# Kernel optimization log

Measured on AMD Instinct MI355X. Metric: run time of the kernel, lower is better.

Reference implementation:

```python
import jax, jax.numpy as jnp
import numpy as np

B, L, H, NH, NB = 16, 200, 128, 2, 2
ITEMS, SPAN = 50000, 256
NEG = -2.0**32 + 1.0  # mask value used by the torch module


def _ln(x, g, b, eps=1e-8):
    m = jnp.mean(x, axis=-1, keepdims=True)
    v = jnp.mean((x - m) ** 2, axis=-1, keepdims=True)
    return (x - m) / jnp.sqrt(v + eps) * g + b


def setup_inputs() -> dict:
    key = jax.random.key(0)
    ks = jax.random.split(key, 20)
    p = lambda k, s: (jax.random.normal(k, s, jnp.float32) * 0.02)
    item_emb = p(ks[0], (ITEMS + 1, H)).at[0].set(0.0)  # padding_idx=0
    return {
        "user_ids": jax.random.randint(ks[1], (B,), 0, 10000),
        "log_seqs": jax.random.randint(ks[2], (B, L), 0, ITEMS),
        "time_matrices": jax.random.randint(ks[3], (B, L, L), 0, SPAN),
        "pos_seqs": jax.random.randint(ks[4], (B, L), 0, ITEMS),
        "neg_seqs": jax.random.randint(ks[5], (B, L), 0, ITEMS),
        "item_emb": item_emb,
        "pos_K_emb": p(ks[6], (L, H)),
        "pos_V_emb": p(ks[7], (L, H)),
        "time_K_emb": p(ks[8], (SPAN + 1, H)),
        "time_V_emb": p(ks[9], (SPAN + 1, H)),
        "Wq": p(ks[10], (NB, H, H)), "bq": jnp.zeros((NB, H)),
        "Wk": p(ks[11], (NB, H, H)), "bk": jnp.zeros((NB, H)),
        "Wv": p(ks[12], (NB, H, H)), "bv": jnp.zeros((NB, H)),
        "ln1_g": jnp.ones((NB, H)), "ln1_b": jnp.zeros((NB, H)),
        "W1": p(ks[13], (NB, H, H)), "b1": jnp.zeros((NB, H)),
        "W2": p(ks[14], (NB, H, H)), "b2": jnp.zeros((NB, H)),
        "ln2_g": jnp.ones((NB, H)), "ln2_b": jnp.zeros((NB, H)),
        "lnf_g": jnp.ones((H,)), "lnf_b": jnp.zeros((H,)),
    }


def reference(user_ids, log_seqs, time_matrices, pos_seqs, neg_seqs,
              item_emb, pos_K_emb, pos_V_emb, time_K_emb, time_V_emb,
              Wq, bq, Wk, bk, Wv, bv, ln1_g, ln1_b,
              W1, b1, W2, b2, ln2_g, ln2_b, lnf_g, lnf_b):
    d = H // NH
    pad = (log_seqs == 0)                    # (B,L) timeline mask
    keep = (~pad)[..., None].astype(jnp.float32)

    seqs = item_emb[log_seqs] * jnp.sqrt(jnp.float32(H))
    seqs = seqs * keep
    posK = pos_K_emb.reshape(L, NH, d)       # same for every batch element
    posV = pos_V_emb.reshape(L, NH, d)
    tmK = time_K_emb[time_matrices].reshape(B, L, L, NH, d)  # (B,L,L,h,d)
    tmV = time_V_emb[time_matrices].reshape(B, L, L, NH, d)
    causal = ~jnp.tril(jnp.ones((L, L), dtype=bool))          # True = masked
    mask = pad[:, None, :, None] | causal[None, None, :, :]   # (B,1,L,L) row-mask | causal

    for i in range(NB):
        Q = (seqs @ Wq[i].T + bq[i]).reshape(B, L, NH, d)
        K = (seqs @ Wk[i].T + bk[i]).reshape(B, L, NH, d)
        V = (seqs @ Wv[i].T + bv[i]).reshape(B, L, NH, d)
        aw = jnp.einsum('bqhd,bkhd->bhqk', Q, K)
        aw = aw + jnp.einsum('bqhd,khd->bhqk', Q, posK)
        aw = aw + jnp.einsum('bqkhd,bqhd->bhqk', tmK, Q)
        aw = aw / jnp.sqrt(jnp.float32(d))
        aw = jnp.where(mask, NEG, aw)
        A = jax.nn.softmax(aw, axis=-1)                        # (B,h,L,L)
        out = jnp.einsum('bhqk,bkhd->bqhd', A, V)
        out = out + jnp.einsum('bhqk,khd->bqhd', A, posV)
        out = out + jnp.einsum('bhqk,bqkhd->bqhd', A, tmV)
        out = out.reshape(B, L, H)
        seqs = _ln(seqs + out, ln1_g[i], ln1_b[i])
        ffn = jax.nn.relu(seqs @ W1[i].T + b1[i]) @ W2[i].T + b2[i]
        seqs = _ln(seqs + ffn, ln2_g[i], ln2_b[i])
        seqs = seqs * keep

    log_feats = _ln(seqs, lnf_g, lnf_b)
    pos_logits = jnp.sum(log_feats * item_emb[pos_seqs], axis=-1)  # (B,L)
    neg_logits = jnp.sum(log_feats * item_emb[neg_seqs], axis=-1)
    return jnp.stack([pos_logits, neg_logits])  # (2,B,L)
```

## Files before the change

### kernel.cpp

```cpp
#include <hip/hip_runtime.h>
#include <hip/hip_bf16.h>
#include <math.h>

#define BB 16
#define LL 200
#define HH 128
#define DD 64
#define NQT 25
#define NEGF -4294967295.0f
#define SQRTH 11.313708498984761f
#define WSTR 129

__device__ __forceinline__ void stage_w(const float* __restrict__ W,
                                        float* __restrict__ w_lds, int t) {
#pragma unroll
    for (int i = 0; i < 8; ++i) {
        int x = t + i * 512;
        int c = x >> 5, k4 = x & 31;
        float4 v = ((const float4*)W)[x];
        float* dst = w_lds + c * WSTR + k4 * 4;
        dst[0] = v.x; dst[1] = v.y; dst[2] = v.z; dst[3] = v.w;
    }
}

__device__ __forceinline__ float wsum64(float v) {
    v += __shfl_xor(v, 1, 64);  v += __shfl_xor(v, 2, 64);
    v += __shfl_xor(v, 4, 64);  v += __shfl_xor(v, 8, 64);
    v += __shfl_xor(v, 16, 64); v += __shfl_xor(v, 32, 64);
    return v;
}

__global__ __launch_bounds__(512) void k_qkv(float* __restrict__ seqs,
    const int* __restrict__ log_seqs, const float* __restrict__ item_emb,
    const float* __restrict__ Wq, const float* __restrict__ bq,
    const float* __restrict__ Wk, const float* __restrict__ bk,
    const float* __restrict__ Wv, const float* __restrict__ bv,
    const float* __restrict__ posK, const float* __restrict__ posV,
    float* __restrict__ Q, float* __restrict__ Kp, float* __restrict__ Vp) {
    __shared__ float s_lds[8][HH];
    __shared__ float w_lds[HH * WSTR];
    int r0g = blockIdx.x * 8;
    int t = threadIdx.x;
    if (t < 256) {
        int r = t >> 5, d4 = t & 31;
        int id = log_seqs[r0g + r];
        float4 v = make_float4(0.f, 0.f, 0.f, 0.f);
        if (id != 0) {
            v = ((const float4*)(item_emb + id * HH))[d4];
            v.x *= SQRTH; v.y *= SQRTH; v.z *= SQRTH; v.w *= SQRTH;
        }
        *(float4*)&s_lds[r][d4 * 4] = v;
        ((float4*)(seqs + r0g * HH))[t] = v;
    }
    stage_w(Wq, w_lds, t);
    __syncthreads();
    int c = t & 127, rg = t >> 7;
    const float* wrow = w_lds + c * WSTR;
    float a0, a1;
    a0 = 0.f; a1 = 0.f;
#pragma unroll 4
    for (int k4 = 0; k4 < 32; ++k4) {
        float w0 = wrow[k4 * 4 + 0], w1 = wrow[k4 * 4 + 1];
        float w2 = wrow[k4 * 4 + 2], w3 = wrow[k4 * 4 + 3];
        float4 s0 = *(const float4*)&s_lds[rg * 2][k4 * 4];
        float4 s1 = *(const float4*)&s_lds[rg * 2 + 1][k4 * 4];
        a0 += s0.x * w0 + s0.y * w1 + s0.z * w2 + s0.w * w3;
        a1 += s1.x * w0 + s1.y * w1 + s1.z * w2 + s1.w * w3;
    }
    Q[(r0g + rg * 2) * HH + c]     = a0 + bq[c];
    Q[(r0g + rg * 2 + 1) * HH + c] = a1 + bq[c];
    __syncthreads();
    stage_w(Wk, w_lds, t);
    __syncthreads();
    a0 = 0.f; a1 = 0.f;
#pragma unroll 4
    for (int k4 = 0; k4 < 32; ++k4) {
        float w0 = wrow[k4 * 4 + 0], w1 = wrow[k4 * 4 + 1];
        float w2 = wrow[k4 * 4 + 2], w3 = wrow[k4 * 4 + 3];
        float4 s0 = *(const float4*)&s_lds[rg * 2][k4 * 4];
        float4 s1 = *(const float4*)&s_lds[rg * 2 + 1][k4 * 4];
        a0 += s0.x * w0 + s0.y * w1 + s0.z * w2 + s0.w * w3;
        a1 += s1.x * w0 + s1.y * w1 + s1.z * w2 + s1.w * w3;
    }
    {
        int row0 = r0g + rg * 2, row1 = row0 + 1;
        Kp[row0 * HH + c] = a0 + bk[c] + posK[(row0 % LL) * HH + c];
        Kp[row1 * HH + c] = a1 + bk[c] + posK[(row1 % LL) * HH + c];
    }
    __syncthreads();
    stage_w(Wv, w_lds, t);
    __syncthreads();
    a0 = 0.f; a1 = 0.f;
#pragma unroll 4
    for (int k4 = 0; k4 < 32; ++k4) {
        float w0 = wrow[k4 * 4 + 0], w1 = wrow[k4 * 4 + 1];
        float w2 = wrow[k4 * 4 + 2], w3 = wrow[k4 * 4 + 3];
        float4 s0 = *(const float4*)&s_lds[rg * 2][k4 * 4];
        float4 s1 = *(const float4*)&s_lds[rg * 2 + 1][k4 * 4];
        a0 += s0.x * w0 + s0.y * w1 + s0.z * w2 + s0.w * w3;
        a1 += s1.x * w0 + s1.y * w1 + s1.z * w2 + s1.w * w3;
    }
    {
        int row0 = r0g + rg * 2, row1 = row0 + 1;
        Vp[row0 * HH + c] = a0 + bv[c] + posV[(row0 % LL) * HH + c];
        Vp[row1 * HH + c] = a1 + bv[c] + posV[(row1 % LL) * HH + c];
    }
}

__global__ __launch_bounds__(256) void k_proj(const float* __restrict__ Q,
    const float* __restrict__ timeK, float* __restrict__ projK) {
    int bh = blockIdx.x / 25, qt = blockIdx.x % 25;
    int b = bh >> 1, h = bh & 1;
    int qlo = qt * 8;
    __shared__ float Qs[8][68];
    __shared__ float TK[32][68];
    int t = threadIdx.x;
    if (t < 128) {
        int r = t >> 4, d4 = t & 15;
        *(float4*)&Qs[r][d4 * 4] =
            ((const float4*)(Q + (b * LL + qlo + r) * HH + h * DD))[d4];
    }
    int tq = t >> 5, ttl = t & 31;
    for (int ch = 0; ch < 9; ++ch) {
        int base = ch * 32;
        __syncthreads();
        for (int x = t; x < 512; x += 256) {
            int i = x >> 4, d4 = x & 15;
            int tt = base + i;
            if (tt < 257)
                *(float4*)&TK[i][d4 * 4] =
                    ((const float4*)(timeK + tt * HH + h * DD))[d4];
        }
        __syncthreads();
        int tt = base + ttl;
        if (tt < 257) {
            float acc = 0.f;
#pragma unroll
            for (int d4 = 0; d4 < 16; ++d4) {
                float4 qv = *(const float4*)&Qs[tq][d4 * 4];
                float4 kv = *(const float4*)&TK[ttl][d4 * 4];
                acc += qv.x * kv.x + qv.y * kv.y + qv.z * kv.z + qv.w * kv.w;
            }
            projK[(bh * LL + qlo + tq) * 257 + tt] = acc;
        }
    }
}

__global__ __launch_bounds__(256) void k_attn(
    const float* __restrict__ Q, const float* __restrict__ Kp, const float* __restrict__ Vp,
    const float* __restrict__ projK, const float* __restrict__ timeV,
    const int* __restrict__ tm, const int* __restrict__ log_seqs,
    float* __restrict__ attnout) {
    int bh = blockIdx.x / NQT, qt = blockIdx.x % NQT;
    int b = bh >> 1, h = bh & 1;
    int qlo = qt * 8;
    __shared__ float K_s[32][68];
    __shared__ float smemW[457 * 12];
    __shared__ int s_allmask;
#define WT(i, j) smemW[(i) * 12 + (j)]
    int t = threadIdx.x;
    int tq = t >> 5, lane = t & 31, g = tq;
    int q = qlo + tq;
    int qhi = qlo + 7;

    if (t == 0) s_allmask = 0;
    for (int x = 200 * 12 + t; x < 457 * 12; x += 256) smemW[x] = 0.f;
    float4 qreg[16];
    {
        const float4* qp = (const float4*)(Q + (b * LL + q) * HH + h * DD);
#pragma unroll
        for (int d4 = 0; d4 < 16; ++d4) qreg[d4] = qp[d4];
    }
    const int* tmrow = tm + (b * LL + q) * LL;
    const float* projrow = projK + (bh * LL + q) * 257;
    const int* lsrow = log_seqs + b * LL;

    float s[7];
#pragma unroll
    for (int j = 0; j < 7; ++j) s[j] = NEGF;
    int nkc = (qhi >> 5) + 1;
#pragma unroll
    for (int kc = 0; kc < 7; ++kc) {
        if (kc < nkc) {
            int kbase = kc * 32;
            for (int x = t; x < 512; x += 256) {
                int i = x >> 4, d4 = x & 15;
                int k = kbase + i;
                if (k < LL)
                    *(float4*)&K_s[i][d4 * 4] =
                        ((const float4*)(Kp + (b * LL + k) * HH + h * DD))[d4];
            }
            __syncthreads();
            int k = kbase + lane;
            if (k <= q && lsrow[k] != 0) {
                float acc = 0.f;
#pragma unroll
                for (int d4 = 0; d4 < 16; ++d4) {
                    float4 kv = *(const float4*)&K_s[lane][d4 * 4];
                    acc += qreg[d4].x * kv.x + qreg[d4].y * kv.y +
                           qreg[d4].z * kv.z + qreg[d4].w * kv.w;
                }
                s[kc] = (acc + projrow[tmrow[k]]) * 0.125f;
            }
            __syncthreads();
        }
    }

    float mx = s[0];
#pragma unroll
    for (int j = 1; j < 7; ++j) mx = fmaxf(mx, s[j]);
    mx = fmaxf(mx, __shfl_xor(mx, 1, 64));
    mx = fmaxf(mx, __shfl_xor(mx, 2, 64));
    mx = fmaxf(mx, __shfl_xor(mx, 4, 64));
    mx = fmaxf(mx, __shfl_xor(mx, 8, 64));
    mx = fmaxf(mx, __shfl_xor(mx, 16, 64));
    bool allmask = (mx == NEGF);
    float sum = 0.f;
#pragma unroll
    for (int j = 0; j < 7; ++j) {
        int k = lane + 32 * j;
        float e = (k < LL) ? __expf(s[j] - mx) : 0.f;
        s[j] = e;
        sum += e;
    }
    sum += __shfl_xor(sum, 1, 64);
    sum += __shfl_xor(sum, 2, 64);
    sum += __shfl_xor(sum, 4, 64);
    sum += __shfl_xor(sum, 8, 64);
    sum += __shfl_xor(sum, 16, 64);
    float inv = 1.0f / sum;
    int klim = allmask ? LL : (q + 1);
    if (allmask && lane == 0) s_allmask = 1;
#pragma unroll
    for (int j = 0; j < 7; ++j) {
        int k = lane + 32 * j;
        if (k < LL) {
            float p = s[j] * inv;
            WT(k, tq) = p;
            if (k < klim && p != 0.f)
                atomicAdd(&WT(200 + tmrow[k], tq), p);
        }
    }
    __syncthreads();

    int kmax = s_allmask ? LL : (qhi + 1);
    float a00=0.f,a01=0.f,a10=0.f,a11=0.f,a20=0.f,a21=0.f,a30=0.f,a31=0.f;
    float a40=0.f,a41=0.f,a50=0.f,a51=0.f,a60=0.f,a61=0.f,a70=0.f,a71=0.f;
#define PV_STEP(WROW, SRCPTR)                                            \
    {                                                                    \
        const float* wr = &WROW;                                         \
        float4 w0 = *(const float4*)wr;                                  \
        float4 w1 = *(const float4*)(wr + 4);                            \
        float2 vv = *(const float2*)(SRCPTR);                            \
        a00 += w0.x * vv.x; a01 += w0.x * vv.y;                          \
        a10 += w0.y * vv.x; a11 += w0.y * vv.y;                          \
        a20 += w0.z * vv.x; a21 += w0.z * vv.y;                          \
        a30 += w0.w * vv.x; a31 += w0.w * vv.y;                          \
        a40 += w1.x * vv.x; a41 += w1.x * vv.y;                          \
        a50 += w1.y * vv.x; a51 += w1.y * vv.y;                          \
        a60 += w1.z * vv.x; a61 += w1.z * vv.y;                          \
        a70 += w1.w * vv.x; a71 += w1.w * vv.y;                          \
    }
    for (int i = g; i < kmax; i += 8)
        PV_STEP(WT(i, 0), Vp + (b * LL + i) * HH + h * DD + lane * 2);
    for (int i = g; i < 257; i += 8)
        PV_STEP(WT(200 + i, 0), timeV + i * HH + h * DD + lane * 2);
#undef PV_STEP
    __syncthreads();
    float* part = smemW;
    part[g * 512 + 0 * 64 + lane * 2] = a00; part[g * 512 + 0 * 64 + lane * 2 + 1] = a01;
    part[g * 512 + 1 * 64 + lane * 2] = a10; part[g * 512 + 1 * 64 + lane * 2 + 1] = a11;
    part[g * 512 + 2 * 64 + lane * 2] = a20; part[g * 512 + 2 * 64 + lane * 2 + 1] = a21;
    part[g * 512 + 3 * 64 + lane * 2] = a30; part[g * 512 + 3 * 64 + lane * 2 + 1] = a31;
    part[g * 512 + 4 * 64 + lane * 2] = a40; part[g * 512 + 4 * 64 + lane * 2 + 1] = a41;
    part[g * 512 + 5 * 64 + lane * 2] = a50; part[g * 512 + 5 * 64 + lane * 2 + 1] = a51;
    part[g * 512 + 6 * 64 + lane * 2] = a60; part[g * 512 + 6 * 64 + lane * 2 + 1] = a61;
    part[g * 512 + 7 * 64 + lane * 2] = a70; part[g * 512 + 7 * 64 + lane * 2 + 1] = a71;
    __syncthreads();
    {
        float ox = 0.f, oy = 0.f;
#pragma unroll
        for (int gg = 0; gg < 8; ++gg) {
            ox += part[gg * 512 + tq * 64 + lane * 2];
            oy += part[gg * 512 + tq * 64 + lane * 2 + 1];
        }
        *(float2*)(attnout + (b * LL + q) * HH + h * DD + lane * 2) =
            make_float2(ox, oy);
    }
#undef WT
}

__global__ __launch_bounds__(512) void k_ffn_full(
    float* __restrict__ seqs, const float* __restrict__ AO,
    const float* __restrict__ g1, const float* __restrict__ be1,
    const float* __restrict__ W1, const float* __restrict__ b1,
    const float* __restrict__ W2, const float* __restrict__ b2,
    const float* __restrict__ g2, const float* __restrict__ be2,
    const int* __restrict__ log_seqs,
    int do_qkv,
    const float* __restrict__ Wq, const float* __restrict__ bq,
    const float* __restrict__ Wk, const float* __restrict__ bk,
    const float* __restrict__ Wv, const float* __restrict__ bv,
    const float* __restrict__ posK, const float* __restrict__ posV,
    float* __restrict__ Q, float* __restrict__ Kp, float* __restrict__ Vp,
    int do_final,
    const float* __restrict__ lnf_g, const float* __restrict__ lnf_b,
    const float* __restrict__ item_emb,
    const int* __restrict__ pos_seqs, const int* __restrict__ neg_seqs,
    float* __restrict__ out) {
    __shared__ float s_lds[8][HH];
    __shared__ float h_lds[8][HH];
    __shared__ float w_lds[HH * WSTR];
    int r0g = blockIdx.x * 8;
    int t = threadIdx.x;
    if (t < 256) {
        float4 a = ((const float4*)(seqs + r0g * HH))[t];
        float4 o = ((const float4*)(AO + r0g * HH))[t];
        a.x += o.x; a.y += o.y; a.z += o.z; a.w += o.w;
        ((float4*)s_lds)[t] = a;
    }
    stage_w(W1, w_lds, t);
    __syncthreads();
    int wv = t >> 6, lane = t & 63;
    {
        float x0 = s_lds[wv][lane], x1 = s_lds[wv][lane + 64];
        float mean = wsum64(x0 + x1) * (1.0f / HH);
        float d0 = x0 - mean, d1 = x1 - mean;
        float var = wsum64(d0 * d0 + d1 * d1) * (1.0f / HH);
        float rstd = rsqrtf(var + 1e-8f);
        s_lds[wv][lane]      = d0 * rstd * g1[lane] + be1[lane];
        s_lds[wv][lane + 64] = d1 * rstd * g1[lane + 64] + be1[lane + 64];
    }
    __syncthreads();
    int c = t & 127, rg = t >> 7;
    const float* wrow = w_lds + c * WSTR;
    float a0, a1;
    a0 = 0.f; a1 = 0.f;
#pragma unroll 4
    for (int k4 = 0; k4 < 32; ++k4) {
        float w0 = wrow[k4 * 4 + 0], w1 = wrow[k4 * 4 + 1];
        float w2 = wrow[k4 * 4 + 2], w3 = wrow[k4 * 4 + 3];
        float4 s0 = *(const float4*)&s_lds[rg * 2][k4 * 4];
        float4 s1 = *(const float4*)&s_lds[rg * 2 + 1][k4 * 4];
        a0 += s0.x * w0 + s0.y * w1 + s0.z * w2 + s0.w * w3;
        a1 += s1.x * w0 + s1.y * w1 + s1.z * w2 + s1.w * w3;
    }
    h_lds[rg * 2][c]     = fmaxf(a0 + b1[c], 0.f);
    h_lds[rg * 2 + 1][c] = fmaxf(a1 + b1[c], 0.f);
    __syncthreads();
    stage_w(W2, w_lds, t);
    __syncthreads();
    a0 = 0.f; a1 = 0.f;
#pragma unroll 4
    for (int k4 = 0; k4 < 32; ++k4) {
        float w0 = wrow[k4 * 4 + 0], w1 = wrow[k4 * 4 + 1];
        float w2 = wrow[k4 * 4 + 2], w3 = wrow[k4 * 4 + 3];
        float4 s0 = *(const float4*)&h_lds[rg * 2][k4 * 4];
        float4 s1 = *(const float4*)&h_lds[rg * 2 + 1][k4 * 4];
        a0 += s0.x * w0 + s0.y * w1 + s0.z * w2 + s0.w * w3;
        a1 += s1.x * w0 + s1.y * w1 + s1.z * w2 + s1.w * w3;
    }
    __syncthreads();
    h_lds[rg * 2][c]     = s_lds[rg * 2][c] + a0 + b2[c];
    h_lds[rg * 2 + 1][c] = s_lds[rg * 2 + 1][c] + a1 + b2[c];
    __syncthreads();
    {
        float x0 = h_lds[wv][lane], x1 = h_lds[wv][lane + 64];
        float mean = wsum64(x0 + x1) * (1.0f / HH);
        float d0 = x0 - mean, d1 = x1 - mean;
        float var = wsum64(d0 * d0 + d1 * d1) * (1.0f / HH);
        float rstd = rsqrtf(var + 1e-8f);
        int row = r0g + wv;
        float keep = (log_seqs[row] != 0) ? 1.0f : 0.0f;
        float y0 = (d0 * rstd * g2[lane] + be2[lane]) * keep;
        float y1 = (d1 * rstd * g2[lane + 64] + be2[lane + 64]) * keep;
        if (do_final) {
            float mean2 = wsum64(y0 + y1) * (1.0f / HH);
            float e0 = y0 - mean2, e1 = y1 - mean2;
            float var2 = wsum64(e0 * e0 + e1 * e1) * (1.0f / HH);
            float rstd2 = rsqrtf(var2 + 1e-8f);
            int pid = pos_seqs[row];
            int nid = neg_seqs[row];
            float lf0 = e0 * rstd2 * lnf_g[lane] + lnf_b[lane];
            float lf1 = e1 * rstd2 * lnf_g[lane + 64] + lnf_b[lane + 64];
            float pp = wsum64(lf0 * item_emb[pid * HH + lane] +
                              lf1 * item_emb[pid * HH + lane + 64]);
            float nn = wsum64(lf0 * item_emb[nid * HH + lane] +
                              lf1 * item_emb[nid * HH + lane + 64]);
            if (lane == 0) {
                out[row] = pp;
                out[BB * LL + row] = nn;
            }
        } else {
            seqs[row * HH + lane]      = y0;
            seqs[row * HH + lane + 64] = y1;
            if (do_qkv) {
                s_lds[wv][lane]      = y0;
                s_lds[wv][lane + 64] = y1;
            }
        }
    }
    if (!do_qkv) return;
    __syncthreads();
    stage_w(Wq, w_lds, t);
    __syncthreads();
    a0 = 0.f; a1 = 0.f;
#pragma unroll 4
    for (int k4 = 0; k4 < 32; ++k4) {
        float w0 = wrow[k4 * 4 + 0], w1 = wrow[k4 * 4 + 1];
        float w2 = wrow[k4 * 4 + 2], w3 = wrow[k4 * 4 + 3];
        float4 s0 = *(const float4*)&s_lds[rg * 2][k4 * 4];
        float4 s1 = *(const float4*)&s_lds[rg * 2 + 1][k4 * 4];
        a0 += s0.x * w0 + s0.y * w1 + s0.z * w2 + s0.w * w3;
        a1 += s1.x * w0 + s1.y * w1 + s1.z * w2 + s1.w * w3;
    }
    Q[(r0g + rg * 2) * HH + c]     = a0 + bq[c];
    Q[(r0g + rg * 2 + 1) * HH + c] = a1 + bq[c];
    __syncthreads();
    stage_w(Wk, w_lds, t);
    __syncthreads();
    a0 = 0.f; a1 = 0.f;
#pragma unroll 4
    for (int k4 = 0; k4 < 32; ++k4) {
        float w0 = wrow[k4 * 4 + 0], w1 = wrow[k4 * 4 + 1];
        float w2 = wrow[k4 * 4 + 2], w3 = wrow[k4 * 4 + 3];
        float4 s0 = *(const float4*)&s_lds[rg * 2][k4 * 4];
        float4 s1 = *(const float4*)&s_lds[rg * 2 + 1][k4 * 4];
        a0 += s0.x * w0 + s0.y * w1 + s0.z * w2 + s0.w * w3;
        a1 += s1.x * w0 + s1.y * w1 + s1.z * w2 + s1.w * w3;
    }
    {
        int row0 = r0g + rg * 2, row1 = row0 + 1;
        Kp[row0 * HH + c] = a0 + bk[c] + posK[(row0 % LL) * HH + c];
        Kp[row1 * HH + c] = a1 + bk[c] + posK[(row1 % LL) * HH + c];
    }
    __syncthreads();
    stage_w(Wv, w_lds, t);
    __syncthreads();
    a0 = 0.f; a1 = 0.f;
#pragma unroll 4
    for (int k4 = 0; k4 < 32; ++k4) {
        float w0 = wrow[k4 * 4 + 0], w1 = wrow[k4 * 4 + 1];
        float w2 = wrow[k4 * 4 + 2], w3 = wrow[k4 * 4 + 3];
        float4 s0 = *(const float4*)&s_lds[rg * 2][k4 * 4];
        float4 s1 = *(const float4*)&s_lds[rg * 2 + 1][k4 * 4];
        a0 += s0.x * w0 + s0.y * w1 + s0.z * w2 + s0.w * w3;
        a1 += s1.x * w0 + s1.y * w1 + s1.z * w2 + s1.w * w3;
    }
    {
        int row0 = r0g + rg * 2, row1 = row0 + 1;
        Vp[row0 * HH + c] = a0 + bv[c] + posV[(row0 % LL) * HH + c];
        Vp[row1 * HH + c] = a1 + bv[c] + posV[(row1 % LL) * HH + c];
    }
}

extern "C" void kernel_launch(void* const* d_in, const int* in_sizes, int n_in,
                              void* d_out, int out_size, void* d_ws, size_t ws_size,
                              hipStream_t stream) {
    const int* log_seqs = (const int*)d_in[1];
    const int* tm       = (const int*)d_in[2];
    const int* pos_seqs = (const int*)d_in[3];
    const int* neg_seqs = (const int*)d_in[4];
    const float* item_emb = (const float*)d_in[5];
    const float* posK   = (const float*)d_in[6];
    const float* posV   = (const float*)d_in[7];
    const float* timeK  = (const float*)d_in[8];
    const float* timeV  = (const float*)d_in[9];
    const float* Wq = (const float*)d_in[10];
    const float* bq = (const float*)d_in[11];
    const float* Wk = (const float*)d_in[12];
    const float* bk = (const float*)d_in[13];
    const float* Wv = (const float*)d_in[14];
    const float* bv = (const float*)d_in[15];
    const float* ln1_g = (const float*)d_in[16];
    const float* ln1_b = (const float*)d_in[17];
    const float* W1 = (const float*)d_in[18];
    const float* b1 = (const float*)d_in[19];
    const float* W2 = (const float*)d_in[20];
    const float* b2 = (const float*)d_in[21];
    const float* ln2_g = (const float*)d_in[22];
    const float* ln2_b = (const float*)d_in[23];
    const float* lnf_g = (const float*)d_in[24];
    const float* lnf_b = (const float*)d_in[25];

    float* ws    = (float*)d_ws;
    float* seqs  = ws;
    float* Qb    = seqs + 409600;
    float* Kpb   = Qb + 409600;
    float* Vpb   = Kpb + 409600;
    float* AO    = Vpb + 409600;
    float* projK = AO + 409600;

    k_qkv<<<BB * LL / 8, 512, 0, stream>>>(seqs, log_seqs, item_emb,
        Wq, bq, Wk, bk, Wv, bv, posK, posV, Qb, Kpb, Vpb);
    k_proj<<<32 * NQT, 256, 0, stream>>>(Qb, timeK, projK);
    k_attn<<<32 * NQT, 256, 0, stream>>>(Qb, Kpb, Vpb, projK, timeV,
                                         tm, log_seqs, AO);
    k_ffn_full<<<BB * LL / 8, 512, 0, stream>>>(seqs, AO,
        ln1_g, ln1_b, W1, b1, W2, b2, ln2_g, ln2_b, log_seqs,
        1, Wq + HH * HH, bq + HH, Wk + HH * HH, bk + HH, Wv + HH * HH, bv + HH,
        posK, posV, Qb, Kpb, Vpb,
        0, lnf_g, lnf_b, item_emb, pos_seqs, neg_seqs, (float*)d_out);
    k_proj<<<32 * NQT, 256, 0, stream>>>(Qb, timeK, projK);
    k_attn<<<32 * NQT, 256, 0, stream>>>(Qb, Kpb, Vpb, projK, timeV,
                                         tm, log_seqs, AO);
    k_ffn_full<<<BB * LL / 8, 512, 0, stream>>>(seqs, AO,
        ln1_g + HH, ln1_b + HH, W1 + HH * HH, b1 + HH, W2 + HH * HH, b2 + HH,
        ln2_g + HH, ln2_b + HH, log_seqs,
        0, nullptr, nullptr, nullptr, nullptr, nullptr, nullptr,
        nullptr, nullptr, nullptr, nullptr, nullptr,
        1, lnf_g, lnf_b, item_emb, pos_seqs, neg_seqs, (float*)d_out);
}
```

Baseline: 166.5 us.

## Double rows per block and prefetch next weight matrix into registers

The QKV and FFN kernels now run 1024-thread blocks covering 16 rows instead of 8, so each staged 128x128 weight matrix in LDS serves twice as many rows. The next weight matrix is loaded from global memory into registers while the current matmul runs, then written to LDS after the barrier, so its load latency overlaps compute. The cost is half as many blocks (200 instead of 400) on a large GPU, which lowers parallelism, plus higher register pressure from the prefetch buffers under the 1024-thread launch bound.

```diff
diff --git a/kernel.cpp b/kernel.cpp
--- a/kernel.cpp
+++ b/kernel.cpp
@@ -14,12 +14,28 @@
 __device__ __forceinline__ void stage_w(const float* __restrict__ W,
                                         float* __restrict__ w_lds, int t) {
 #pragma unroll
-    for (int i = 0; i < 8; ++i) {
-        int x = t + i * 512;
+    for (int i = 0; i < 4; ++i) {
+        int x = t + i * 1024;
         int c = x >> 5, k4 = x & 31;
         float4 v = ((const float4*)W)[x];
         float* dst = w_lds + c * WSTR + k4 * 4;
         dst[0] = v.x; dst[1] = v.y; dst[2] = v.z; dst[3] = v.w;
+    }
+}
+
+__device__ __forceinline__ void prefetch_w(const float* __restrict__ W,
+                                           float4* __restrict__ r, int t) {
+#pragma unroll
+    for (int i = 0; i < 4; ++i) r[i] = ((const float4*)W)[t + i * 1024];
+}
+__device__ __forceinline__ void commit_w(const float4* __restrict__ r,
+                                         float* __restrict__ w_lds, int t) {
+#pragma unroll
+    for (int i = 0; i < 4; ++i) {
+        int x = t + i * 1024;
+        int c = x >> 5, k4 = x & 31;
+        float* dst = w_lds + c * WSTR + k4 * 4;
+        dst[0] = r[i].x; dst[1] = r[i].y; dst[2] = r[i].z; dst[3] = r[i].w;
     }
 }
 
@@ -30,18 +46,18 @@
     return v;
 }
 
-__global__ __launch_bounds__(512) void k_qkv(float* __restrict__ seqs,
+__global__ __launch_bounds__(1024) void k_qkv(float* __restrict__ seqs,
     const int* __restrict__ log_seqs, const float* __restrict__ item_emb,
     const float* __restrict__ Wq, const float* __restrict__ bq,
     const float* __restrict__ Wk, const float* __restrict__ bk,
     const float* __restrict__ Wv, const float* __restrict__ bv,
     const float* __restrict__ posK, const float* __restrict__ posV,
     float* __restrict__ Q, float* __restrict__ Kp, float* __restrict__ Vp) {
-    __shared__ float s_lds[8][HH];
+    __shared__ float s_lds[16][HH];
     __shared__ float w_lds[HH * WSTR];
-    int r0g = blockIdx.x * 8;
+    int r0g = blockIdx.x * 16;
     int t = threadIdx.x;
-    if (t < 256) {
+    if (t < 512) {
         int r = t >> 5, d4 = t & 31;
         int id = log_seqs[r0g + r];
         float4 v = make_float4(0.f, 0.f, 0.f, 0.f);
@@ -57,6 +73,8 @@
     int c = t & 127, rg = t >> 7;
     const float* wrow = w_lds + c * WSTR;
     float a0, a1;
+    float4 pw[4];
+    prefetch_w(Wk, pw, t);
     a0 = 0.f; a1 = 0.f;
 #pragma unroll 4
     for (int k4 = 0; k4 < 32; ++k4) {
@@ -70,8 +88,9 @@
     Q[(r0g + rg * 2) * HH + c]     = a0 + bq[c];
     Q[(r0g + rg * 2 + 1) * HH + c] = a1 + bq[c];
     __syncthreads();
-    stage_w(Wk, w_lds, t);
-    __syncthreads();
+    commit_w(pw, w_lds, t);
+    __syncthreads();
+    prefetch_w(Wv, pw, t);
     a0 = 0.f; a1 = 0.f;
 #pragma unroll 4
     for (int k4 = 0; k4 < 32; ++k4) {
@@ -88,7 +107,7 @@
         Kp[row1 * HH + c] = a1 + bk[c] + posK[(row1 % LL) * HH + c];
     }
     __syncthreads();
-    stage_w(Wv, w_lds, t);
+    commit_w(pw, w_lds, t);
     __syncthreads();
     a0 = 0.f; a1 = 0.f;
 #pragma unroll 4
@@ -290,7 +309,7 @@
 #undef WT
 }
 
-__global__ __launch_bounds__(512) void k_ffn_full(
+__global__ __launch_bounds__(1024) void k_ffn_full(
     float* __restrict__ seqs, const float* __restrict__ AO,
     const float* __restrict__ g1, const float* __restrict__ be1,
     const float* __restrict__ W1, const float* __restrict__ b1,
@@ -308,12 +327,12 @@
     const float* __restrict__ item_emb,
     const int* __restrict__ pos_seqs, const int* __restrict__ neg_seqs,
     float* __restrict__ out) {
-    __shared__ float s_lds[8][HH];
-    __shared__ float h_lds[8][HH];
+    __shared__ float s_lds[16][HH];
+    __shared__ float h_lds[16][HH];
     __shared__ float w_lds[HH * WSTR];
-    int r0g = blockIdx.x * 8;
+    int r0g = blockIdx.x * 16;
     int t = threadIdx.x;
-    if (t < 256) {
+    if (t < 512) {
         float4 a = ((const float4*)(seqs + r0g * HH))[t];
         float4 o = ((const float4*)(AO + r0g * HH))[t];
         a.x += o.x; a.y += o.y; a.z += o.z; a.w += o.w;
@@ -335,6 +354,8 @@
     int c = t & 127, rg = t >> 7;
     const float* wrow = w_lds + c * WSTR;
     float a0, a1;
+    float4 pw[4];
+    prefetch_w(W2, pw, t);
     a0 = 0.f; a1 = 0.f;
 #pragma unroll 4
     for (int k4 = 0; k4 < 32; ++k4) {
@@ -348,8 +369,9 @@
     h_lds[rg * 2][c]     = fmaxf(a0 + b1[c], 0.f);
     h_lds[rg * 2 + 1][c] = fmaxf(a1 + b1[c], 0.f);
     __syncthreads();
-    stage_w(W2, w_lds, t);
-    __syncthreads();
+    commit_w(pw, w_lds, t);
+    __syncthreads();
+    if (do_qkv) prefetch_w(Wq, pw, t);
     a0 = 0.f; a1 = 0.f;
 #pragma unroll 4
     for (int k4 = 0; k4 < 32; ++k4) {
@@ -402,8 +424,9 @@
     }
     if (!do_qkv) return;
     __syncthreads();
-    stage_w(Wq, w_lds, t);
-    __syncthreads();
+    commit_w(pw, w_lds, t);
+    __syncthreads();
+    prefetch_w(Wk, pw, t);
     a0 = 0.f; a1 = 0.f;
 #pragma unroll 4
     for (int k4 = 0; k4 < 32; ++k4) {
@@ -417,8 +440,9 @@
     Q[(r0g + rg * 2) * HH + c]     = a0 + bq[c];
     Q[(r0g + rg * 2 + 1) * HH + c] = a1 + bq[c];
     __syncthreads();
-    stage_w(Wk, w_lds, t);
-    __syncthreads();
+    commit_w(pw, w_lds, t);
+    __syncthreads();
+    prefetch_w(Wv, pw, t);
     a0 = 0.f; a1 = 0.f;
 #pragma unroll 4
     for (int k4 = 0; k4 < 32; ++k4) {
@@ -435,7 +459,7 @@
         Kp[row1 * HH + c] = a1 + bk[c] + posK[(row1 % LL) * HH + c];
     }
     __syncthreads();
-    stage_w(Wv, w_lds, t);
+    commit_w(pw, w_lds, t);
     __syncthreads();
     a0 = 0.f; a1 = 0.f;
 #pragma unroll 4
@@ -491,12 +515,12 @@
     float* AO    = Vpb + 409600;
     float* projK = AO + 409600;
 
-    k_qkv<<<BB * LL / 8, 512, 0, stream>>>(seqs, log_seqs, item_emb,
+    k_qkv<<<BB * LL / 16, 1024, 0, stream>>>(seqs, log_seqs, item_emb,
         Wq, bq, Wk, bk, Wv, bv, posK, posV, Qb, Kpb, Vpb);
     k_proj<<<32 * NQT, 256, 0, stream>>>(Qb, timeK, projK);
     k_attn<<<32 * NQT, 256, 0, stream>>>(Qb, Kpb, Vpb, projK, timeV,
                                          tm, log_seqs, AO);
-    k_ffn_full<<<BB * LL / 8, 512, 0, stream>>>(seqs, AO,
+    k_ffn_full<<<BB * LL / 16, 1024, 0, stream>>>(seqs, AO,
         ln1_g, ln1_b, W1, b1, W2, b2, ln2_g, ln2_b, log_seqs,
         1, Wq + HH * HH, bq + HH, Wk + HH * HH, bk + HH, Wv + HH * HH, bv + HH,
         posK, posV, Qb, Kpb, Vpb,
@@ -504,7 +528,7 @@
     k_proj<<<32 * NQT, 256, 0, stream>>>(Qb, timeK, projK);
     k_attn<<<32 * NQT, 256, 0, stream>>>(Qb, Kpb, Vpb, projK, timeV,
                                          tm, log_seqs, AO);
-    k_ffn_full<<<BB * LL / 8, 512, 0, stream>>>(seqs, AO,
+    k_ffn_full<<<BB * LL / 16, 1024, 0, stream>>>(seqs, AO,
         ln1_g + HH, ln1_b + HH, W1 + HH * HH, b1 + HH, W2 + HH * HH, b2 + HH,
         ln2_g + HH, ln2_b + HH, log_seqs,
         0, nullptr, nullptr, nullptr, nullptr, nullptr, nullptr,
```

Result: faster. 160.6 us (median of 3 runs) (-3.6%).
